# Kernel tuning notes

Hardware: AMD Instinct MI355X
Metric: run time of the kernel (lower is better)

Reference implementation:

```python
import jax, jax.numpy as jnp
import numpy as np

D = 512      # Config.vector_sizes[1]
S = 1024     # Config.sequence_lengths[1]
B = 16       # read batch
Q = 64       # Config.use_pndb1
NDOCS = 8    # external A-matrix memory slots
NL = 2       # encoder layers


def rope(x):
    # rotary position embedding over last dim, x: [b, s, d]
    s, d = x.shape[-2], x.shape[-1]
    inv = 1.0 / (10000.0 ** (jnp.arange(0, d, 2, dtype=jnp.float32) / d))
    ang = jnp.arange(s, dtype=jnp.float32)[:, None] * inv[None, :]  # [s, d/2]
    sin, cos = jnp.sin(ang), jnp.cos(ang)
    x1, x2 = x[..., ::2], x[..., 1::2]
    out = jnp.stack([x1 * cos - x2 * sin, x1 * sin + x2 * cos], axis=-1)
    return out.reshape(x.shape)


def layer_norm(x, g, b):
    m = x.mean(-1, keepdims=True)
    v = ((x - m) ** 2).mean(-1, keepdims=True)
    return (x - m) / jnp.sqrt(v + 1e-5) * g + b


def encoder(x, bias, Wqkv, bqkv, Wo, bo, ln, Wff, bff):
    # post-norm transformer encoder, 1 head, rotary on q/k, additive key bias
    d = x.shape[-1]
    scale = 1.0 / jnp.sqrt(jnp.float32(d))
    for l in range(NL):
        q = rope(x @ Wqkv[l, 0] + bqkv[l, 0])
        k = rope(x @ Wqkv[l, 1] + bqkv[l, 1])
        v = x @ Wqkv[l, 2] + bqkv[l, 2]
        scores = jnp.einsum('bqd,bkd->bqk', q, k) * scale + bias[:, None, :]
        a = jax.nn.softmax(scores, axis=-1)
        o = jnp.einsum('bqk,bkd->bqd', a, v) @ Wo[l] + bo[l]
        x = layer_norm(x + o, ln[l, 0, 0], ln[l, 0, 1])
        f = jax.nn.gelu(x @ Wff[l, 0] + bff[l, 0]) @ Wff[l, 1] + bff[l, 1]
        x = layer_norm(x + f, ln[l, 1, 0], ln[l, 1, 1])
    return x


def setup_inputs() -> dict:
    key = jax.random.key(0)
    ks = jax.random.split(key, 24)
    def n(k, shape, s=0.02):
        return jax.random.normal(k, shape, jnp.float32) * s
    ln_init = jnp.tile(jnp.stack([jnp.ones(D), jnp.zeros(D)]), (NL, 2, 1, 1))  # [NL,2,2,D]
    return {
        'raw_emb': jax.random.normal(ks[0], (NDOCS, S, D), jnp.float32),
        'real_pos_write': jax.random.uniform(ks[1], (NDOCS, S), jnp.float32, 0.05, 0.95),
        'post_dec': jax.random.normal(ks[2], (B, S, D), jnp.float32),
        'real_pos_read': jax.random.uniform(ks[4], (B, S), jnp.float32, 0.05, 0.95),
        'questions': jax.random.uniform(ks[5], (Q, D), jnp.float32),
        'W_k': n(ks[6], (D, D)),
        'W_ig': n(ks[7], (D, 1)), 'b_ig': jnp.zeros((1,)),
        'W_u1': n(ks[8], (D, 1)), 'b_u1': jnp.zeros((1,)),
        'W_u2': n(ks[9], (D, 1)), 'b_u2': jnp.zeros((1,)),
        'b1': jax.random.uniform(ks[10], (1,), jnp.float32),
        'W_ok': n(ks[11], (D, D)), 'b_ok': jnp.zeros((D,)),
        'encw_Wqkv': n(ks[12], (NL, 3, D, D)), 'encw_bqkv': jnp.zeros((NL, 3, D)),
        'encw_Wo': n(ks[13], (NL, D, D)), 'encw_bo': jnp.zeros((NL, D)),
        'encw_ln': ln_init,
        'encw_Wff': n(ks[14], (NL, 2, D, D)), 'encw_bff': jnp.zeros((NL, 2, D)),
        'encr_Wqkv': n(ks[15], (NL, 3, D, D)), 'encr_bqkv': jnp.zeros((NL, 3, D)),
        'encr_Wo': n(ks[16], (NL, D, D)), 'encr_bo': jnp.zeros((NL, D)),
        'encr_ln': ln_init,
        'encr_Wff': n(ks[17], (NL, 2, D, D)), 'encr_bff': jnp.zeros((NL, 2, D)),
        'lookup_ids': jax.random.randint(ks[3], (B,), 0, NDOCS, jnp.int32),
    }


def reference(raw_emb, real_pos_write, post_dec, real_pos_read, questions,
              W_k, W_ig, b_ig, W_u1, b_u1, W_u2, b_u2, b1, W_ok, b_ok,
              encw_Wqkv, encw_bqkv, encw_Wo, encw_bo, encw_ln, encw_Wff, encw_bff,
              encr_Wqkv, encr_bqkv, encr_Wo, encr_bo, encr_ln, encr_Wff, encr_bff,
              lookup_ids):
    # ---- create_A_matrix (write path), one A per document ----
    log_pw = jnp.log(real_pos_write)                       # additive key mask
    k = raw_emb @ W_k                                      # to_k (no bias)
    for_ignore = encoder(raw_emb, log_pw, encw_Wqkv, encw_bqkv, encw_Wo,
                         encw_bo, encw_ln, encw_Wff, encw_bff)
    v = raw_emb * jax.nn.sigmoid(for_ignore @ W_ig + b_ig)  # ignore gate
    scores = jnp.einsum('qd,nsd->nqs', questions, k) / jnp.sqrt(jnp.float32(D))
    scores = scores + log_pw[:, None, :]
    A1s = jnp.einsum('nqs,nsd->nqd', jax.nn.softmax(scores, -1), v)  # [NDOCS,Q,D]

    # ---- get_data_from_A_matrix (read path) ----
    logit_pr = jnp.log(real_pos_read) - jnp.log1p(-real_pos_read)  # prob_to_logit
    for_update = encoder(post_dec, logit_pr, encr_Wqkv, encr_bqkv, encr_Wo,
                         encr_bo, encr_ln, encr_Wff, encr_bff)
    k2 = post_dec @ W_ok + b_ok                            # to_output_k
    selA = A1s[lookup_ids]                                 # index_select gather [B,Q,D]
    a2 = jax.nn.softmax(jnp.einsum('bsd,qd->bsq', k2, questions)
                        / jnp.sqrt(jnp.float32(Q)), -1)
    A2 = jnp.einsum('bsq,bqd->bsd', a2, selA)              # [B,S,D]
    gate = jax.nn.sigmoid(for_update @ W_u1 + b_u1 + A2 @ W_u2 + b_u2 + b1 - 4.0)
    out = post_dec * (1.0 - gate) + A2 * gate
    return out, gate
```

## Files before the change

### kernel.cpp

```cpp
#include <hip/hip_runtime.h>
#include <hip/hip_bf16.h>
#include <math.h>

typedef __attribute__((ext_vector_type(8))) short short8;
typedef __attribute__((ext_vector_type(4))) float f32x4;
typedef unsigned short ushortT;

__device__ __forceinline__ unsigned short f2b(float f) {
  union { float f; unsigned u; } v; v.f = f;
  return (unsigned short)((v.u + 0x7FFFu + ((v.u >> 16) & 1u)) >> 16);
}
__device__ __forceinline__ float b2f(unsigned short h) {
  union { unsigned u; float f; } v; v.u = ((unsigned)h) << 16;
  return v.f;
}
__device__ __forceinline__ float gelu_f(float x) {
  return 0.5f * x * (1.0f + tanhf(0.7978845608028654f * (x + 0.044715f * x * x * x)));
}

__device__ __forceinline__ void async16(ushortT* lds, const ushortT* g) {
  __builtin_amdgcn_global_load_lds(
      (const __attribute__((address_space(1))) void*)g,
      (__attribute__((address_space(3))) void*)lds, 16, 0, 0);
}

template<int EMODE>
__global__ __launch_bounds__(256, 3)
void gemm_f(const ushortT* __restrict__ A, const ushortT* __restrict__ Bt,
            const ushortT* __restrict__ A2, const ushortT* __restrict__ Bt2,
            ushortT* __restrict__ C, ushortT* __restrict__ C2,
            const float* __restrict__ bias, const float* __restrict__ bias2,
            int zsplit, int bmode, float scale, long bstride,
            int K, int lda, int ldb, int ldc,
            long sA, long sB, long sC, const float2* __restrict__ tab)
{
  __shared__ ushortT lds[3][2][128 * 32];
  const int gx = gridDim.x, gy = gridDim.y;
  int flat = blockIdx.x + gx * (blockIdx.y + gy * blockIdx.z);
  const int nwg = gx * gy * gridDim.z;
  if ((nwg & 7) == 0) {
    const int per = nwg >> 3;
    flat = (flat & 7) * per + (flat >> 3);
  }
  const int gxy = gx * gy;
  const int z = flat / gxy;
  const int rem = flat - z * gxy;
  const int bm = (rem / gx) * 128, bn = (rem % gx) * 128;

  int zz = z;
  const ushortT* Ap = A; const ushortT* Bp = Bt; const float* bp = bias;
  if (z >= zsplit) { Ap = A2; Bp = Bt2; bp = bias2; zz = z - zsplit; }
  Ap += (long)zz * sA;
  Bp += (long)zz * sB;
  const long coff = (long)z * sC;
  const int tid = threadIdx.x, wave = tid >> 6, lane = tid & 63;
  const int wm = (wave >> 1) << 6, wn = (wave & 1) << 6;
  const int l15 = lane & 15, quad = lane >> 4;

  const ushortT* gA[2]; const ushortT* gB[2];
  int lchunk[2];
#pragma unroll
  for (int q = 0; q < 2; ++q) {
    int r = 32 * wave + 16 * q + (lane >> 2);
    int sw = (((lane & 3) ^ ((r >> 1) & 3)) << 3);
    gA[q] = Ap + (long)(bm + r) * lda + sw;
    gB[q] = Bp + (long)(bn + r) * ldb + sw;
    lchunk[q] = (wave * 2 + q) * 512;
  }

  f32x4 acc[4][4];
#pragma unroll
  for (int i = 0; i < 4; ++i)
#pragma unroll
    for (int j = 0; j < 4; ++j) acc[i][j] = (f32x4){0.f, 0.f, 0.f, 0.f};

  const int x0 = (l15 >> 1) & 3;
  const int nk = K >> 5;

#pragma unroll
  for (int q = 0; q < 2; ++q) {
    async16(&lds[0][0][lchunk[q]], gA[q]);
    async16(&lds[0][1][lchunk[q]], gB[q]);
  }
#pragma unroll
  for (int q = 0; q < 2; ++q) {
    async16(&lds[1][0][lchunk[q]], gA[q] + 32);
    async16(&lds[1][1][lchunk[q]], gB[q] + 32);
  }

  int rb_ = 0, sb_ = 2;
  for (int k = 0; k < nk; ++k) {
    if (k + 2 < nk) {
      int k0 = (k + 2) << 5;
#pragma unroll
      for (int q = 0; q < 2; ++q) {
        async16(&lds[sb_][0][lchunk[q]], gA[q] + k0);
        async16(&lds[sb_][1][lchunk[q]], gB[q] + k0);
      }
    }
    if (k + 2 < nk)      asm volatile("s_waitcnt vmcnt(8)" ::: "memory");
    else if (k + 1 < nk) asm volatile("s_waitcnt vmcnt(4)" ::: "memory");
    else                 asm volatile("s_waitcnt vmcnt(0)" ::: "memory");
    __builtin_amdgcn_s_barrier();
    asm volatile("" ::: "memory");

    short8 aF[4], bF[4];
#pragma unroll
    for (int t = 0; t < 4; ++t) {
      int ra = (wm + t * 16 + l15) << 5;
      aF[t] = *(const short8*)&lds[rb_][0][ra + ((quad ^ x0) << 3)];
      int rbo = (wn + t * 16 + l15) << 5;
      bF[t] = *(const short8*)&lds[rb_][1][rbo + ((quad ^ x0) << 3)];
    }
#pragma unroll
    for (int i = 0; i < 4; ++i)
#pragma unroll
      for (int j = 0; j < 4; ++j)
        acc[i][j] = __builtin_amdgcn_mfma_f32_16x16x32_bf16(aF[i], bF[j], acc[i][j], 0, 0, 0);

    asm volatile("s_waitcnt lgkmcnt(0)" ::: "memory");
    __builtin_amdgcn_s_barrier();
    asm volatile("" ::: "memory");
    rb_ = (rb_ == 2) ? 0 : rb_ + 1;
    sb_ = (sb_ == 2) ? 0 : sb_ + 1;
  }
  __syncthreads();

  ushortT* ct = &lds[0][0][0];
  const float* bz = bp + (long)zz * bstride;
#pragma unroll
  for (int j = 0; j < 4; ++j) {
    int tcol = wn + j * 16 + l15;
    float cbv = (bmode == 1) ? bz[bn + tcol] : 0.0f;
#pragma unroll
    for (int i = 0; i < 4; ++i) {
      int row0 = wm + i * 16 + (quad << 2);
#pragma unroll
      for (int r = 0; r < 4; ++r) {
        int row = row0 + r;
        float bv = (bmode == 2) ? bz[bm + row] : cbv;
        float v = acc[i][j][r] * scale + bv;
        if (EMODE == 1) v = gelu_f(v);
        ct[(row << 7) + tcol] = f2b(v);
      }
    }
  }
  __syncthreads();

  if (EMODE == 2) {
    const bool isq = (bn < 512);
    ushortT* dbase = isq ? C : C2;
    const int cbase = isq ? bn : bn - 512;
#pragma unroll
    for (int it = 0; it < 8; ++it) {
      int trow = it * 16 + (tid >> 4);
      int tcol = (tid & 15) << 3;
      uint4 u = *(const uint4*)&ct[(trow << 7) + tcol];
      int grow = bm + trow;
      int pos = grow & 1023;
      int pair0 = (cbase + tcol) >> 1;
      const float2* tp = &tab[(pos << 8) + pair0];
      unsigned w[4] = {u.x, u.y, u.z, u.w};
      uint4 o;
      unsigned* op = (unsigned*)&o;
#pragma unroll
      for (int p = 0; p < 4; ++p) {
        float2 sc = tp[p];
        float x1 = b2f((ushortT)(w[p] & 0xFFFFu));
        float x2 = b2f((ushortT)(w[p] >> 16));
        float o1 = x1 * sc.y - x2 * sc.x;
        float o2 = x1 * sc.x + x2 * sc.y;
        op[p] = (unsigned)f2b(o1) | ((unsigned)f2b(o2) << 16);
      }
      *(uint4*)&dbase[coff + (long)grow * 512 + cbase + tcol] = o;
    }
  } else {
#pragma unroll
    for (int it = 0; it < 8; ++it) {
      int trow = it * 16 + (tid >> 4);
      int tcol = (tid & 15) << 3;
      *(uint4*)&C[coff + (long)(bm + trow) * ldc + bn + tcol] =
          *(const uint4*)&ct[(trow << 7) + tcol];
    }
  }
}

__global__ void btrans(const ushortT* __restrict__ in, ushortT* __restrict__ out,
                       int R, int C, long ibs, const int* __restrict__ gather) {
  __shared__ float tile[32][33];
  int z = blockIdx.z;
  long ib = (long)(gather ? gather[z] : z) * ibs;
  long ob = (long)z * (long)R * C;
  int c0 = blockIdx.x << 5, r0 = blockIdx.y << 5;
  int tx = threadIdx.x, ty = threadIdx.y;
#pragma unroll
  for (int dy = 0; dy < 32; dy += 8)
    tile[ty + dy][tx] = b2f(in[ib + (long)(r0 + ty + dy) * C + c0 + tx]);
  __syncthreads();
#pragma unroll
  for (int dy = 0; dy < 32; dy += 8)
    out[ob + (long)(c0 + ty + dy) * R + r0 + tx] = f2b(tile[tx][ty + dy]);
}

struct WSrc { const float* p[8]; int c[8]; };
__global__ void wtrans_all(WSrc ws, ushortT* __restrict__ out) {
  __shared__ float tile[32][33];
  int z = blockIdx.z;
  int g = 0, base = 0;
  while (z - base >= ws.c[g]) { base += ws.c[g]; ++g; }
  const float* src = ws.p[g] + (size_t)(z - base) * 262144;
  ushortT* dst = out + (size_t)z * 262144;
  int c0 = blockIdx.x << 5, r0 = blockIdx.y << 5;
  int tx = threadIdx.x, ty = threadIdx.y;
#pragma unroll
  for (int dy = 0; dy < 32; dy += 8)
    tile[ty + dy][tx] = src[(long)(r0 + ty + dy) * 512 + c0 + tx];
  __syncthreads();
#pragma unroll
  for (int dy = 0; dy < 32; dy += 8)
    dst[(long)(c0 + ty + dy) * 512 + r0 + tx] = f2b(tile[tx][ty + dy]);
}

__device__ __forceinline__ void conv4(const float4* in, uint2* out, long i) {
  float4 v = in[i];
  uint2 r;
  r.x = (unsigned)f2b(v.x) | ((unsigned)f2b(v.y) << 16);
  r.y = (unsigned)f2b(v.z) | ((unsigned)f2b(v.w) << 16);
  out[i] = r;
}
__global__ __launch_bounds__(256)
void setup_k(const float* __restrict__ rpw, const float* __restrict__ rpr,
             const float* __restrict__ questions, const float* __restrict__ raw,
             const float* __restrict__ pd,
             float* __restrict__ pbw, float* __restrict__ pbr, float2* __restrict__ tab,
             uint2* __restrict__ qsb, uint2* __restrict__ rab, uint2* __restrict__ pdb,
             float* __restrict__ zb) {
  int b = blockIdx.x, t = threadIdx.x;
  if (b < 32) { int i = b * 256 + t; float v = rpw[i]; pbw[i] = __logf(v); return; }
  b -= 32;
  if (b < 64) { int i = b * 256 + t; float v = rpr[i]; pbr[i] = __logf(v) - log1pf(-v); return; }
  b -= 64;
  if (b < 1024) {
    float inv = __expf(-(float)t * 0.035977892078032f);
    float s, c;
    sincosf((float)b * inv, &s, &c);
    tab[(b << 8) + t] = make_float2(s, c);
    return;
  }
  b -= 1024;
  if (b < 32) { conv4((const float4*)questions, qsb, (long)b * 256 + t); return; }
  b -= 32;
  if (b < 4096) { conv4((const float4*)raw, rab, (long)b * 256 + t); return; }
  b -= 4096;
  if (b < 8192) { conv4((const float4*)pd, pdb, (long)b * 256 + t); return; }
  b -= 8192;
  zb[b * 256 + t] = 0.0f;
}

__global__ __launch_bounds__(256)
void softmax1024(ushortT* __restrict__ x) {
  __shared__ float sred[8];
  int row = blockIdx.x, tid = threadIdx.x, wave = tid >> 6, lane = tid & 63;
  ushortT* xr = x + (long)row * 1024;
  uint2 u = ((const uint2*)xr)[tid];
  float t0 = b2f((ushortT)(u.x & 0xFFFFu));
  float t1 = b2f((ushortT)(u.x >> 16));
  float t2 = b2f((ushortT)(u.y & 0xFFFFu));
  float t3 = b2f((ushortT)(u.y >> 16));
  float m = fmaxf(fmaxf(t0, t1), fmaxf(t2, t3));
  for (int o = 32; o; o >>= 1) m = fmaxf(m, __shfl_xor(m, o));
  if (lane == 0) sred[wave] = m;
  __syncthreads();
  m = fmaxf(fmaxf(sred[0], sred[1]), fmaxf(sred[2], sred[3]));
  float e0 = __expf(t0 - m), e1 = __expf(t1 - m), e2 = __expf(t2 - m), e3 = __expf(t3 - m);
  float s = e0 + e1 + e2 + e3;
  for (int o = 32; o; o >>= 1) s += __shfl_xor(s, o);
  if (lane == 0) sred[4 + wave] = s;
  __syncthreads();
  float inv = 1.0f / (sred[4] + sred[5] + sred[6] + sred[7]);
  uint2 r;
  r.x = (unsigned)f2b(e0 * inv) | ((unsigned)f2b(e1 * inv) << 16);
  r.y = (unsigned)f2b(e2 * inv) | ((unsigned)f2b(e3 * inv) << 16);
  ((uint2*)xr)[tid] = r;
}

__global__ __launch_bounds__(256)
void softmax64(ushortT* __restrict__ x, int ldr) {
  int row = blockIdx.x * 4 + (threadIdx.x >> 6), lane = threadIdx.x & 63;
  ushortT* xr = x + (long)row * ldr;
  float t = b2f(xr[lane]);
  float m = t;
  for (int o = 32; o; o >>= 1) m = fmaxf(m, __shfl_xor(m, o));
  float e = __expf(t - m), s = e;
  for (int o = 32; o; o >>= 1) s += __shfl_xor(s, o);
  xr[lane] = f2b(e / s);
}

__global__ __launch_bounds__(256)
void ln_k(const ushortT* __restrict__ src, const ushortT* __restrict__ res,
          const float* __restrict__ gamma, const float* __restrict__ beta,
          const float* __restrict__ gamma2, const float* __restrict__ beta2,
          int rsplit, ushortT* __restrict__ dst) {
  __shared__ float2 sred[4];
  int row = blockIdx.x, tid = threadIdx.x, wave = tid >> 6, lane = tid & 63;
  const float* gp = gamma; const float* bp = beta;
  if (row >= rsplit) { gp = gamma2; bp = beta2; }
  long off = (long)row * 512;
  float a = b2f(src[off + tid]) + b2f(res[off + tid]);
  float b = b2f(src[off + tid + 256]) + b2f(res[off + tid + 256]);
  float s = a + b, q = a * a + b * b;
  for (int o = 32; o; o >>= 1) { s += __shfl_xor(s, o); q += __shfl_xor(q, o); }
  if (lane == 0) sred[wave] = make_float2(s, q);
  __syncthreads();
  float ts = sred[0].x + sred[1].x + sred[2].x + sred[3].x;
  float tq = sred[0].y + sred[1].y + sred[2].y + sred[3].y;
  float mean = ts * (1.0f / 512.0f);
  float var = tq * (1.0f / 512.0f) - mean * mean;
  float rstd = rsqrtf(fmaxf(var, 0.f) + 1e-5f);
  dst[off + tid]       = f2b((a - mean) * rstd * gp[tid]       + bp[tid]);
  dst[off + tid + 256] = f2b((b - mean) * rstd * gp[tid + 256] + bp[tid + 256]);
}

__global__ __launch_bounds__(256)
void gatev_k(const ushortT* __restrict__ fi, const float* __restrict__ raw,
             const float* __restrict__ wig, const float* __restrict__ big,
             ushortT* __restrict__ vout) {
  __shared__ float sred[4];
  int row = blockIdx.x, tid = threadIdx.x, wave = tid >> 6, lane = tid & 63;
  long off = (long)row * 512;
  float d = b2f(fi[off + tid]) * wig[tid] + b2f(fi[off + tid + 256]) * wig[tid + 256];
  for (int o = 32; o; o >>= 1) d += __shfl_xor(d, o);
  if (lane == 0) sred[wave] = d;
  __syncthreads();
  float g = 1.0f / (1.0f + __expf(-(sred[0] + sred[1] + sred[2] + sred[3] + big[0])));
  vout[off + tid]       = f2b(raw[off + tid] * g);
  vout[off + tid + 256] = f2b(raw[off + tid + 256] * g);
}

__global__ __launch_bounds__(256)
void final_k(const ushortT* __restrict__ fu, const ushortT* __restrict__ A2,
             const float* __restrict__ pd, const float* __restrict__ wu1,
             const float* __restrict__ wu2, const float* __restrict__ bu1,
             const float* __restrict__ bu2, const float* __restrict__ b1p,
             float* __restrict__ outx, float* __restrict__ outg) {
  __shared__ float2 sred[4];
  int row = blockIdx.x, tid = threadIdx.x, wave = tid >> 6, lane = tid & 63;
  long off = (long)row * 512;
  float a2a = b2f(A2[off + tid]), a2b = b2f(A2[off + tid + 256]);
  float d1 = b2f(fu[off + tid]) * wu1[tid] + b2f(fu[off + tid + 256]) * wu1[tid + 256];
  float d2 = a2a * wu2[tid] + a2b * wu2[tid + 256];
  for (int o = 32; o; o >>= 1) { d1 += __shfl_xor(d1, o); d2 += __shfl_xor(d2, o); }
  if (lane == 0) sred[wave] = make_float2(d1, d2);
  __syncthreads();
  float t1 = sred[0].x + sred[1].x + sred[2].x + sred[3].x;
  float t2 = sred[0].y + sred[1].y + sred[2].y + sred[3].y;
  float g = 1.0f / (1.0f + __expf(-(t1 + t2 + bu1[0] + bu2[0] + b1p[0] - 4.0f)));
  outx[off + tid]       = pd[off + tid] * (1.0f - g) + a2a * g;
  outx[off + tid + 256] = pd[off + tid + 256] * (1.0f - g) + a2b * g;
  if (tid == 0) outg[row] = g;
}

extern "C" void kernel_launch(void* const* d_in, const int* in_sizes, int n_in,
                              void* d_out, int out_size, void* d_ws, size_t ws_size,
                              hipStream_t stream)
{
  const float* raw_emb = (const float*)d_in[0];
  const float* rpw     = (const float*)d_in[1];
  const float* post_dec= (const float*)d_in[2];
  const float* rpr     = (const float*)d_in[3];
  const float* questions=(const float*)d_in[4];
  const float* W_k  = (const float*)d_in[5];
  const float* W_ig = (const float*)d_in[6];
  const float* b_ig = (const float*)d_in[7];
  const float* W_u1 = (const float*)d_in[8];
  const float* b_u1 = (const float*)d_in[9];
  const float* W_u2 = (const float*)d_in[10];
  const float* b_u2 = (const float*)d_in[11];
  const float* b1   = (const float*)d_in[12];
  const float* W_ok = (const float*)d_in[13];
  const float* b_ok = (const float*)d_in[14];
  const float* ew_qkv = (const float*)d_in[15];
  const float* ew_bqkv= (const float*)d_in[16];
  const float* ew_wo  = (const float*)d_in[17];
  const float* ew_bo  = (const float*)d_in[18];
  const float* ew_ln  = (const float*)d_in[19];
  const float* ew_wff = (const float*)d_in[20];
  const float* ew_bff = (const float*)d_in[21];
  const float* er_qkv = (const float*)d_in[22];
  const float* er_bqkv= (const float*)d_in[23];
  const float* er_wo  = (const float*)d_in[24];
  const float* er_bo  = (const float*)d_in[25];
  const float* er_ln  = (const float*)d_in[26];
  const float* er_wff = (const float*)d_in[27];
  const float* er_bff = (const float*)d_in[28];
  const int* lookup   = (const int*)d_in[29];

  const size_t MAT = 512ull * 512ull;
  const long SD = 1024l * 512;
  const long SZ = 8192l * 512;
  const int BIGZ = 1 << 28;
  char* wsb = (char*)d_ws;
  size_t off = 0;
  auto alloc = [&](size_t b) { char* p = wsb + off; off = (off + b + 255) & ~(size_t)255; return p; };

  ushortT* WT  = (ushortT*)alloc(26 * MAT * 2);
  ushortT* RAB = (ushortT*)alloc(8192ull * 512 * 2);
  ushortT* PDB = (ushortT*)alloc(16384ull * 512 * 2);
  ushortT* XC  = (ushortT*)alloc(24576ull * 512 * 2);
  ushortT* B1  = (ushortT*)alloc(24576ull * 512 * 2);
  ushortT* SC  = (ushortT*)alloc(24ull * 1024 * 1024 * 2);
  ushortT* QB  = (ushortT*)alloc(24576ull * 512 * 2);
  ushortT* KB  = (ushortT*)alloc(24576ull * 512 * 2);
  ushortT* VT  = (ushortT*)alloc(24ull * 512 * 1024 * 2);
  ushortT* KD2 = (ushortT*)alloc(24576ull * 512 * 2);
  ushortT* QSB = (ushortT*)alloc(128ull * 512 * 2);
  ushortT* SC2 = (ushortT*)alloc(16384ull * 128 * 2);
  ushortT* A1S = (ushortT*)alloc(8ull * 128 * 512 * 2);
  ushortT* SAT = (ushortT*)alloc(16ull * 512 * 64 * 2);
  float*   PBW = (float*)alloc(8192 * 4);
  float*   PBR = (float*)alloc(16384 * 4);
  float2*  TAB = (float2*)alloc(1024 * 256 * 8);
  float*   ZB  = (float*)alloc(512 * 4);

  auto gemm = [&](int emode, const ushortT* A, const ushortT* Bt,
                  const ushortT* A2p, const ushortT* Bt2p,
                  ushortT* C, ushortT* C2,
                  const float* bias, const float* bias2, int zsplit,
                  int bmode, float scale, long bstride,
                  int M, int N, int K, int lda, int ldb, int ldc,
                  int Z, long sA, long sB, long sC) {
    dim3 g(N / 128, M / 128, Z);
    if (emode == 0)
      gemm_f<0><<<g, dim3(256), 0, stream>>>(A, Bt, A2p, Bt2p, C, nullptr, bias, bias2,
                                             zsplit, bmode, scale, bstride,
                                             K, lda, ldb, ldc, sA, sB, sC, TAB);
    else if (emode == 1)
      gemm_f<1><<<g, dim3(256), 0, stream>>>(A, Bt, A2p, Bt2p, C, nullptr, bias, bias2,
                                             zsplit, bmode, scale, bstride,
                                             K, lda, ldb, ldc, sA, sB, sC, TAB);
    else
      gemm_f<2><<<g, dim3(256), 0, stream>>>(A, Bt, A2p, Bt2p, C, C2, bias, bias2,
                                             zsplit, bmode, scale, bstride,
                                             K, lda, ldb, ldc, sA, sB, sC, TAB);
  };

  const float isc512 = 0.044194173824159216f;

  WSrc wsrc;
  wsrc.p[0] = W_k;    wsrc.c[0] = 1;
  wsrc.p[1] = W_ok;   wsrc.c[1] = 1;
  wsrc.p[2] = ew_qkv; wsrc.c[2] = 6;
  wsrc.p[3] = ew_wo;  wsrc.c[3] = 2;
  wsrc.p[4] = ew_wff; wsrc.c[4] = 4;
  wsrc.p[5] = er_qkv; wsrc.c[5] = 6;
  wsrc.p[6] = er_wo;  wsrc.c[6] = 2;
  wsrc.p[7] = er_wff; wsrc.c[7] = 4;
  wtrans_all<<<dim3(16, 16, 26), dim3(32, 8), 0, stream>>>(wsrc, WT);
  setup_k<<<13442, 256, 0, stream>>>(rpw, rpr, questions, raw_emb, post_dec,
                                     PBW, PBR, TAB, (uint2*)QSB, (uint2*)RAB, (uint2*)PDB, ZB);

  gemm(0, RAB, WT + 0 * MAT, RAB + SZ, WT + 1 * MAT, KD2, nullptr,
       ZB, b_ok, 1, 1, 1.0f, 0,
       8192, 512, 512, 512, 512, 512, 3, SZ, 0, SZ);

  for (int l = 0; l < 2; ++l) {
    const ushortT* xs = (l == 0) ? RAB : XC;
    const ushortT* WqkW = WT + (size_t)(2 + l * 3) * MAT;
    const ushortT* WqkR = WT + (size_t)(14 + l * 3) * MAT;
    const ushortT* WvW  = WT + (size_t)(4 + l * 3) * MAT;
    const ushortT* WvR  = WT + (size_t)(16 + l * 3) * MAT;
    const ushortT* WoW  = WT + (size_t)(8 + l) * MAT;
    const ushortT* WoR  = WT + (size_t)(20 + l) * MAT;
    const ushortT* Wf0W = WT + (size_t)(10 + l * 2) * MAT;
    const ushortT* Wf0R = WT + (size_t)(22 + l * 2) * MAT;
    const ushortT* Wf1W = WT + (size_t)(11 + l * 2) * MAT;
    const ushortT* Wf1R = WT + (size_t)(23 + l * 2) * MAT;

    gemm(2, xs, WqkW, xs + SZ, WqkR, QB, KB,
         ew_bqkv + (l * 3) * 512, er_bqkv + (l * 3) * 512, 1,
         1, 1.0f, 0,
         8192, 1024, 512, 512, 512, 512, 3, SZ, 0, SZ);
    gemm(0, WvW, xs, WvR, xs + 8 * SD, VT, nullptr,
         ew_bqkv + (l * 3 + 2) * 512, er_bqkv + (l * 3 + 2) * 512, 8,
         2, 1.0f, 0,
         512, 1024, 512, 512, 512, 1024, 24, 0, SD, SD);
    gemm(0, QB, KB, QB, KB, SC, nullptr,
         PBW, PBW, BIGZ, 1, isc512, 1024,
         1024, 1024, 512, 512, 512, 1024, 24, SD, SD, 1024l * 1024);
    softmax1024<<<24576, 256, 0, stream>>>(SC);
    gemm(0, SC, VT, SC, VT, QB, nullptr,
         nullptr, nullptr, BIGZ, 0, 1.0f, 0,
         1024, 512, 1024, 1024, 1024, 512, 24, 1024l * 1024, SD, SD);
    gemm(0, QB, WoW, QB + SZ, WoR, B1, nullptr,
         ew_bo + l * 512, er_bo + l * 512, 1, 1, 1.0f, 0,
         8192, 512, 512, 512, 512, 512, 3, SZ, 0, SZ);
    ln_k<<<24576, 256, 0, stream>>>(xs, B1,
         ew_ln + (l * 4 + 0) * 512, ew_ln + (l * 4 + 1) * 512,
         er_ln + (l * 4 + 0) * 512, er_ln + (l * 4 + 1) * 512, 8192, XC);
    gemm(1, XC, Wf0W, XC + SZ, Wf0R, KB, nullptr,
         ew_bff + (l * 2) * 512, er_bff + (l * 2) * 512, 1, 1, 1.0f, 0,
         8192, 512, 512, 512, 512, 512, 3, SZ, 0, SZ);
    gemm(0, KB, Wf1W, KB + SZ, Wf1R, B1, nullptr,
         ew_bff + (l * 2 + 1) * 512, er_bff + (l * 2 + 1) * 512, 1, 1, 1.0f, 0,
         8192, 512, 512, 512, 512, 512, 3, SZ, 0, SZ);
    ln_k<<<24576, 256, 0, stream>>>(XC, B1,
         ew_ln + (l * 4 + 2) * 512, ew_ln + (l * 4 + 3) * 512,
         er_ln + (l * 4 + 2) * 512, er_ln + (l * 4 + 3) * 512, 8192, XC);
  }

  gatev_k<<<8192, 256, 0, stream>>>(XC, raw_emb, W_ig, b_ig, B1);
  btrans<<<dim3(16, 32, 8), dim3(32, 8), 0, stream>>>(B1, VT, 1024, 512, SD, nullptr);
  gemm(0, QSB, KD2, QSB, KD2, SC2, nullptr,
       PBW, PBW, BIGZ, 1, isc512, 1024,
       128, 1024, 512, 512, 512, 1024, 8, 0, SD, 128l * 1024);
  softmax1024<<<1024, 256, 0, stream>>>(SC2);
  gemm(0, SC2, VT, SC2, VT, A1S, nullptr,
       nullptr, nullptr, BIGZ, 0, 1.0f, 0,
       128, 512, 1024, 1024, 1024, 512, 8, 128l * 1024, SD, 128l * 512);

  gemm(0, KD2 + SZ, QSB, KD2 + SZ, QSB, SC2, nullptr,
       nullptr, nullptr, BIGZ, 0, 0.125f, 0,
       16384, 128, 512, 512, 512, 128, 1, 0, 0, 0);
  softmax64<<<4096, 256, 0, stream>>>(SC2, 128);
  btrans<<<dim3(16, 2, 16), dim3(32, 8), 0, stream>>>(A1S, SAT, 64, 512, 128 * 512, lookup);
  gemm(0, SC2, SAT, SC2, SAT, QB, nullptr,
       nullptr, nullptr, BIGZ, 0, 1.0f, 0,
       1024, 512, 64, 128, 64, 512, 16, 1024l * 128, 512l * 64, SD);

  float* outp = (float*)d_out;
  final_k<<<16384, 256, 0, stream>>>(XC + SZ, QB, post_dec, W_u1, W_u2, b_u1, b_u2, b1,
                                     outp, outp + 8388608);
}
```

Before: 836.5 us.

## Add 256x256-tile, 8-wave GEMM kernel for tile-divisible shapes

Adds a second GEMM kernel that computes a 256x256 output tile per workgroup with 512 threads (8 waves, each handling 128x64). It uses a double-buffered async global-to-LDS pipeline and writes the epilogue through LDS in two column halves. Shapes divisible by 256 are sent to it, and the rest still use the 128x128 kernel. The aim is more operand reuse per LDS load and less global traffic. In exchange it launches fewer workgroups, which can leave CUs idle on the smaller GEMMs, and it raises register pressure from 32 accumulator fragments per wave.

```diff
diff --git a/kernel.cpp b/kernel.cpp
--- a/kernel.cpp
+++ b/kernel.cpp
@@ -22,6 +22,167 @@
   __builtin_amdgcn_global_load_lds(
       (const __attribute__((address_space(1))) void*)g,
       (__attribute__((address_space(3))) void*)lds, 16, 0, 0);
+}
+
+template<int EMODE>
+__global__ __launch_bounds__(512, 2)
+void gemm8(const ushortT* __restrict__ A, const ushortT* __restrict__ Bt,
+           const ushortT* __restrict__ A2, const ushortT* __restrict__ Bt2,
+           ushortT* __restrict__ C, ushortT* __restrict__ C2,
+           const float* __restrict__ bias, const float* __restrict__ bias2,
+           int zsplit, int bmode, float scale, long bstride,
+           int K, int lda, int ldb, int ldc,
+           long sA, long sB, long sC, const float2* __restrict__ tab)
+{
+  __shared__ ushortT lds[2][2][256 * 32];
+  const int gx = gridDim.x, gy = gridDim.y;
+  int flat = blockIdx.x + gx * (blockIdx.y + gy * blockIdx.z);
+  const int nwg = gx * gy * gridDim.z;
+  if ((nwg & 7) == 0) { const int per = nwg >> 3; flat = (flat & 7) * per + (flat >> 3); }
+  const int gxy = gx * gy;
+  const int z = flat / gxy;
+  const int rem = flat - z * gxy;
+  const int bm = (rem / gx) * 256, bn = (rem % gx) * 256;
+
+  int zz = z;
+  const ushortT* Ap = A; const ushortT* Bp = Bt; const float* bp = bias;
+  if (z >= zsplit) { Ap = A2; Bp = Bt2; bp = bias2; zz = z - zsplit; }
+  Ap += (long)zz * sA;
+  Bp += (long)zz * sB;
+  const long coff = (long)z * sC;
+  const int tid = threadIdx.x, wave = tid >> 6, lane = tid & 63;
+  const int wm = (wave >> 2) << 7;
+  const int wn = (wave & 3) << 6;
+  const int l15 = lane & 15, quad = lane >> 4;
+  const int x0 = (l15 >> 1) & 3;
+
+  const ushortT* gA[2]; const ushortT* gB[2]; int lodst[2];
+#pragma unroll
+  for (int q = 0; q < 2; ++q) {
+    int r = q * 128 + (tid >> 2);
+    int sw = ((tid & 3) ^ ((r >> 1) & 3)) << 3;
+    gA[q] = Ap + (long)(bm + r) * lda + sw;
+    gB[q] = Bp + (long)(bn + r) * ldb + sw;
+    lodst[q] = q * 4096 + tid * 8;
+  }
+
+  f32x4 acc[8][4];
+#pragma unroll
+  for (int i = 0; i < 8; ++i)
+#pragma unroll
+    for (int j = 0; j < 4; ++j) acc[i][j] = (f32x4){0.f, 0.f, 0.f, 0.f};
+
+  const int nk = K >> 5;
+
+#pragma unroll
+  for (int q = 0; q < 2; ++q) {
+    async16(&lds[0][0][lodst[q]], gA[q]);
+    async16(&lds[0][1][lodst[q]], gB[q]);
+  }
+#pragma unroll
+  for (int q = 0; q < 2; ++q) {
+    async16(&lds[1][0][lodst[q]], gA[q] + 32);
+    async16(&lds[1][1][lodst[q]], gB[q] + 32);
+  }
+  asm volatile("s_waitcnt vmcnt(4)" ::: "memory");
+  __builtin_amdgcn_s_barrier();
+
+  int cur = 0;
+  for (int t = 0; t < nk; ++t) {
+    short8 bF[4];
+#pragma unroll
+    for (int j = 0; j < 4; ++j)
+      bF[j] = *(const short8*)&lds[cur][1][((wn + j * 16 + l15) << 5) + ((quad ^ x0) << 3)];
+    __builtin_amdgcn_s_setprio(1);
+#pragma unroll
+    for (int i = 0; i < 8; ++i) {
+      short8 aF = *(const short8*)&lds[cur][0][((wm + i * 16 + l15) << 5) + ((quad ^ x0) << 3)];
+#pragma unroll
+      for (int j = 0; j < 4; ++j)
+        acc[i][j] = __builtin_amdgcn_mfma_f32_16x16x32_bf16(aF, bF[j], acc[i][j], 0, 0, 0);
+    }
+    __builtin_amdgcn_s_setprio(0);
+    asm volatile("s_waitcnt lgkmcnt(0)" ::: "memory");
+    __builtin_amdgcn_s_barrier();
+    if (t + 2 < nk) {
+      int k0 = (t + 2) << 5;
+#pragma unroll
+      for (int q = 0; q < 2; ++q) {
+        async16(&lds[cur][0][lodst[q]], gA[q] + k0);
+        async16(&lds[cur][1][lodst[q]], gB[q] + k0);
+      }
+      asm volatile("s_waitcnt vmcnt(4)" ::: "memory");
+    } else if (t + 1 < nk) {
+      asm volatile("s_waitcnt vmcnt(0)" ::: "memory");
+    }
+    __builtin_amdgcn_s_barrier();
+    cur ^= 1;
+  }
+  __syncthreads();
+
+  ushortT* ct = &lds[0][0][0];
+  const float* bz = bp + (long)zz * bstride;
+#pragma unroll
+  for (int h = 0; h < 2; ++h) {
+    if (((wave >> 1) & 1) == h) {
+      const int wnl = (wave & 1) << 6;
+#pragma unroll
+      for (int j = 0; j < 4; ++j) {
+        int tcl = wnl + j * 16 + l15;
+        float cbv = (bmode == 1) ? bz[bn + h * 128 + tcl] : 0.0f;
+#pragma unroll
+        for (int i = 0; i < 8; ++i) {
+          int row0 = wm + i * 16 + (quad << 2);
+#pragma unroll
+          for (int r = 0; r < 4; ++r) {
+            int row = row0 + r;
+            float bv = (bmode == 2) ? bz[bm + row] : cbv;
+            float v = acc[i][j][r] * scale + bv;
+            if (EMODE == 1) v = gelu_f(v);
+            ct[(row << 7) + tcl] = f2b(v);
+          }
+        }
+      }
+    }
+    __syncthreads();
+    if (EMODE == 2) {
+      const int gcb = bn + h * 128;
+      const bool isq = gcb < 512;
+      ushortT* dbase = isq ? C : C2;
+      const int cb2 = isq ? gcb : gcb - 512;
+#pragma unroll
+      for (int it = 0; it < 8; ++it) {
+        int trow = it * 32 + (tid >> 4);
+        int tcl = (tid & 15) << 3;
+        uint4 u = *(const uint4*)&ct[(trow << 7) + tcl];
+        int grow = bm + trow;
+        int pos = grow & 1023;
+        int pair0 = (cb2 + tcl) >> 1;
+        const float2* tp = &tab[(pos << 8) + pair0];
+        unsigned w[4] = {u.x, u.y, u.z, u.w};
+        uint4 o; unsigned* op = (unsigned*)&o;
+#pragma unroll
+        for (int p = 0; p < 4; ++p) {
+          float2 sc = tp[p];
+          float xx1 = b2f((ushortT)(w[p] & 0xFFFFu));
+          float xx2 = b2f((ushortT)(w[p] >> 16));
+          float o1 = xx1 * sc.y - xx2 * sc.x;
+          float o2 = xx1 * sc.x + xx2 * sc.y;
+          op[p] = (unsigned)f2b(o1) | ((unsigned)f2b(o2) << 16);
+        }
+        *(uint4*)&dbase[coff + (long)grow * 512 + cb2 + tcl] = o;
+      }
+    } else {
+#pragma unroll
+      for (int it = 0; it < 8; ++it) {
+        int trow = it * 32 + (tid >> 4);
+        int tcl = (tid & 15) << 3;
+        *(uint4*)&C[coff + (long)(bm + trow) * ldc + bn + h * 128 + tcl] =
+            *(const uint4*)&ct[(trow << 7) + tcl];
+      }
+    }
+    __syncthreads();
+  }
 }
 
 template<int EMODE>
@@ -429,19 +590,35 @@
                   int bmode, float scale, long bstride,
                   int M, int N, int K, int lda, int ldb, int ldc,
                   int Z, long sA, long sB, long sC) {
-    dim3 g(N / 128, M / 128, Z);
-    if (emode == 0)
-      gemm_f<0><<<g, dim3(256), 0, stream>>>(A, Bt, A2p, Bt2p, C, nullptr, bias, bias2,
-                                             zsplit, bmode, scale, bstride,
-                                             K, lda, ldb, ldc, sA, sB, sC, TAB);
-    else if (emode == 1)
-      gemm_f<1><<<g, dim3(256), 0, stream>>>(A, Bt, A2p, Bt2p, C, nullptr, bias, bias2,
-                                             zsplit, bmode, scale, bstride,
-                                             K, lda, ldb, ldc, sA, sB, sC, TAB);
-    else
-      gemm_f<2><<<g, dim3(256), 0, stream>>>(A, Bt, A2p, Bt2p, C, C2, bias, bias2,
-                                             zsplit, bmode, scale, bstride,
-                                             K, lda, ldb, ldc, sA, sB, sC, TAB);
+    if ((M % 256 == 0) && (N % 256 == 0)) {
+      dim3 g(N / 256, M / 256, Z);
+      if (emode == 0)
+        gemm8<0><<<g, dim3(512), 0, stream>>>(A, Bt, A2p, Bt2p, C, nullptr, bias, bias2,
+                                              zsplit, bmode, scale, bstride,
+                                              K, lda, ldb, ldc, sA, sB, sC, TAB);
+      else if (emode == 1)
+        gemm8<1><<<g, dim3(512), 0, stream>>>(A, Bt, A2p, Bt2p, C, nullptr, bias, bias2,
+                                              zsplit, bmode, scale, bstride,
+                                              K, lda, ldb, ldc, sA, sB, sC, TAB);
+      else
+        gemm8<2><<<g, dim3(512), 0, stream>>>(A, Bt, A2p, Bt2p, C, C2, bias, bias2,
+                                              zsplit, bmode, scale, bstride,
+                                              K, lda, ldb, ldc, sA, sB, sC, TAB);
+    } else {
+      dim3 g(N / 128, M / 128, Z);
+      if (emode == 0)
+        gemm_f<0><<<g, dim3(256), 0, stream>>>(A, Bt, A2p, Bt2p, C, nullptr, bias, bias2,
+                                               zsplit, bmode, scale, bstride,
+                                               K, lda, ldb, ldc, sA, sB, sC, TAB);
+      else if (emode == 1)
+        gemm_f<1><<<g, dim3(256), 0, stream>>>(A, Bt, A2p, Bt2p, C, nullptr, bias, bias2,
+                                               zsplit, bmode, scale, bstride,
+                                               K, lda, ldb, ldc, sA, sB, sC, TAB);
+      else
+        gemm_f<2><<<g, dim3(256), 0, stream>>>(A, Bt, A2p, Bt2p, C, C2, bias, bias2,
+                                               zsplit, bmode, scale, bstride,
+                                               K, lda, ldb, ldc, sA, sB, sC, TAB);
+    }
   };
 
   const float isc512 = 0.044194173824159216f;
```

New measurement: 1.097 ms. 1.31x slower.
